# Optimization experiments

Hardware: AMD Instinct MI355X
Metric: run time of the kernel (lower is better)

The kernel has to match this reference:

```python
import jax, jax.numpy as jnp
import numpy as np

EPS = 1e-8

def _apply_norms(x):
    # x: [B, C, H, W]; torch .std() is unbiased (ddof=1)
    x_min = x.min(axis=1, keepdims=True)
    x_max = x.max(axis=1, keepdims=True)
    norm_minmax = (x - x_min) / (x_max - x_min + EPS)
    x_mean = x.mean(axis=1, keepdims=True)
    x_std = x.std(axis=1, keepdims=True, ddof=1)
    norm_z = (x - x_mean) / (x_std + EPS)
    b_mean = x.mean(axis=(0, 2, 3), keepdims=True)
    b_std = x.std(axis=(0, 2, 3), keepdims=True, ddof=1)
    norm_bn = (x - b_mean) / (b_std + EPS)
    return [norm_minmax, norm_z, norm_bn]

def _compute_metrics(pred, targ):
    B, C, H, W = pred.shape
    p = pred.reshape(B, C, H * W)
    t = targ.reshape(B, C, H * W)
    # SAM: 1 - cosine similarity over channel dim (torch clamps norms at eps)
    dot = (p * t).sum(axis=1)
    np_ = jnp.maximum(jnp.sqrt((p * p).sum(axis=1)), EPS)
    nt_ = jnp.maximum(jnp.sqrt((t * t).sum(axis=1)), EPS)
    sam = 1.0 - dot / (np_ * nt_)
    # Pearson over channel dim
    p_ctr = p - p.mean(axis=1, keepdims=True)
    t_ctr = t - t.mean(axis=1, keepdims=True)
    cov = (p_ctr * t_ctr).sum(axis=1)
    std_p = jnp.sqrt((p_ctr ** 2).sum(axis=1) + EPS)
    std_t = jnp.sqrt((t_ctr ** 2).sum(axis=1) + EPS)
    pearson = 1.0 - cov / (std_p * std_t)
    # SID: symmetric KL over channel-normalized positive distributions
    p_pos = p - p.min(axis=1, keepdims=True)
    t_pos = t - t.min(axis=1, keepdims=True)
    p_prob = jnp.maximum(p_pos / (p_pos.sum(axis=1, keepdims=True) + EPS), EPS)
    t_prob = jnp.maximum(t_pos / (t_pos.sum(axis=1, keepdims=True) + EPS), EPS)
    log_ratio = jnp.log(p_prob / t_prob)
    d_pt = (p_prob * log_ratio).sum(axis=1)
    d_tp = (t_prob * (-log_ratio)).sum(axis=1)
    sid = d_pt + d_tp
    return sam, pearson, sid  # each [B, H*W]

TOP_K_RATIO = 0.05

def setup_inputs() -> dict:
    key = jax.random.key(0)
    k1, k2 = jax.random.split(key)
    B, C, H, W = 4, 128, 256, 256
    reconstructed = jax.random.normal(k1, (B, C, H, W), dtype=jnp.float32)
    target = jax.random.normal(k2, (B, C, H, W), dtype=jnp.float32)
    loss_weights = jnp.ones((9,), dtype=jnp.float32)
    return {"reconstructed": reconstructed, "target": target, "loss_weights": loss_weights}

def reference(reconstructed, target, loss_weights):
    B, C, H, W = reconstructed.shape
    preds = _apply_norms(reconstructed)
    targs = _apply_norms(target)
    all_losses = []
    for p_norm, t_norm in zip(preds, targs):
        sam, pearson, sid = _compute_metrics(p_norm, t_norm)
        all_losses.extend([sam, pearson, sid])
    stacked = jnp.stack(all_losses, axis=0)  # [9, B, H*W]
    weights = jax.nn.softmax(loss_weights).reshape(9, 1, 1)
    weighted_error_map = (stacked * weights).sum(axis=0)  # [B, H*W]
    err_flat = weighted_error_map.reshape(-1)
    k = max(1, int(err_flat.shape[0] * TOP_K_RATIO))
    top_k_errors, _ = jax.lax.top_k(err_flat, k)
    return jnp.mean(top_k_errors), weighted_error_map.reshape(B, H, W)
```

## Files before the change

### kernel.cpp

```cpp
#include <hip/hip_runtime.h>

#define EPSF 1e-8f
#define CCH 128
#define HWSZ 65536
#define NPIX 262144
#define KTOP 13107
#define LN2F 0.6931471805599453f

#define WS_CST    512
#define WS_WGT    1024
#define WS_MINKEY 1040
#define WS_MAXKEY 1041
#define WS_BSTAR  1042
#define WS_CNTAB  1043
#define WS_LO2    1044
#define WS_W2     1045
#define WS_K2     1046
#define WS_SUMAB  1048
#define WS_H1     1056
#define WS_H2C    5152
#define WS_H2S    9248
#define WS_TOTAL  13344

__device__ __forceinline__ unsigned fkey(float f){
  unsigned u = __float_as_uint(f);
  return (u & 0x80000000u) ? ~u : (u | 0x80000000u);
}
__device__ __forceinline__ float funkey(unsigned k){
  unsigned u = (k & 0x80000000u) ? (k & 0x7fffffffu) : ~k;
  return __uint_as_float(u);
}

struct Stats {
  float psum,psumsq,tsum,tsumsq,ptsum,pmin,pmax,tmin,tmax;
  float bS1,bS11,bS2,bS22,bS12,bMp,bMt;
};
struct Consts { float errBase,fp,Bp,ft,Bt,fbp,Bbp,fbt,Bbt,sidW,bnW; };

__device__ Consts pixEpilogue(const Stats& s, const float* wgt){
  const float Ci = 1.0f/128.0f;
  float smm_p = 1.f/(s.pmax-s.pmin+EPSF);
  float smm_t = 1.f/(s.tmax-s.tmin+EPSF);
  float mean_p = s.psum*Ci, mean_t = s.tsum*Ci;
  float var_p = fmaxf((s.psumsq - s.psum*s.psum*Ci)*(1.f/127.f), 0.f);
  float var_t = fmaxf((s.tsumsq - s.tsum*s.tsum*Ci)*(1.f/127.f), 0.f);
  float zi_p = 1.f/(sqrtf(var_p)+EPSF);
  float zi_t = 1.f/(sqrtf(var_t)+EPSF);

  auto metrics = [&](float S1,float S11,float S2,float S22,float S12,
                     float& sam,float& pear){
    float npn = fmaxf(sqrtf(fmaxf(S11,0.f)), EPSF);
    float ntn = fmaxf(sqrtf(fmaxf(S22,0.f)), EPSF);
    sam = 1.f - S12/(npn*ntn);
    float cov = S12 - S1*S2*Ci;
    float vp = fmaxf(S11 - S1*S1*Ci, 0.f);
    float vt = fmaxf(S22 - S2*S2*Ci, 0.f);
    pear = 1.f - cov/(sqrtf(vp+EPSF)*sqrtf(vt+EPSF));
  };
  auto affine = [&](float ap,float sp,float at,float st,float& sam,float& pear){
    float S1 = (s.psum - 128.f*ap)*sp;
    float S11 = (s.psumsq - 2.f*ap*s.psum + 128.f*ap*ap)*sp*sp;
    float S2 = (s.tsum - 128.f*at)*st;
    float S22 = (s.tsumsq - 2.f*at*s.tsum + 128.f*at*at)*st*st;
    float S12 = (s.ptsum - at*s.psum - ap*s.tsum + 128.f*ap*at)*sp*st;
    metrics(S1,S11,S2,S22,S12,sam,pear);
  };

  float sam_mm,pear_mm,sam_z,pear_z,sam_bn,pear_bn;
  affine(s.pmin,smm_p,s.tmin,smm_t,sam_mm,pear_mm);
  affine(mean_p,zi_p,mean_t,zi_t,sam_z,pear_z);
  metrics(s.bS1,s.bS11,s.bS2,s.bS22,s.bS12,sam_bn,pear_bn);

  Consts c;
  c.errBase = wgt[0]*sam_mm + wgt[1]*pear_mm + wgt[3]*sam_z + wgt[4]*pear_z
            + wgt[6]*sam_bn + wgt[7]*pear_bn;
  float dp = fmaf(s.psum - 128.f*s.pmin, smm_p, EPSF);
  c.fp = smm_p/dp;  c.Bp = s.pmin*c.fp;
  float dt = fmaf(s.tsum - 128.f*s.tmin, smm_t, EPSF);
  c.ft = smm_t/dt;  c.Bt = s.tmin*c.ft;
  c.fbp = 1.f/((s.bS1 - 128.f*s.bMp) + EPSF); c.Bbp = s.bMp*c.fbp;
  c.fbt = 1.f/((s.bS2 - 128.f*s.bMt) + EPSF); c.Bbt = s.bMt*c.fbt;
  c.sidW = (wgt[2]+wgt[5])*LN2F;
  c.bnW  = wgt[8]*LN2F;
  return c;
}

__global__ __launch_bounds__(256) void initWs(unsigned* __restrict__ wsu){
  int idx = blockIdx.x*256 + threadIdx.x;
  if (idx < WS_TOTAL) wsu[idx] = (idx == WS_MINKEY) ? 0xFFFFFFFFu : 0u;
}

__global__ __launch_bounds__(256) void streamStatsKernel(const float* __restrict__ rec,
                                                         const float* __restrict__ tgt,
                                                         float* __restrict__ wsf){
  __shared__ float ws_[4], wq_[4];
  int tid = threadIdx.x;
  for (int ch = blockIdx.x; ch < 16384; ch += 2048){
    int tensor = ch >> 13;
    int ci = ch & 8191;
    const float4* base = (const float4*)(tensor ? tgt : rec) + (size_t)ci*1024;
    float4 L0 = base[tid];
    float4 L1 = base[tid + 256];
    float4 L2 = base[tid + 512];
    float4 L3 = base[tid + 768];
    float s = ((L0.x+L0.y)+(L0.z+L0.w)) + ((L1.x+L1.y)+(L1.z+L1.w))
            + ((L2.x+L2.y)+(L2.z+L2.w)) + ((L3.x+L3.y)+(L3.z+L3.w));
    float q = (fmaf(L0.x,L0.x,L0.y*L0.y) + fmaf(L0.z,L0.z,L0.w*L0.w))
            + (fmaf(L1.x,L1.x,L1.y*L1.y) + fmaf(L1.z,L1.z,L1.w*L1.w))
            + (fmaf(L2.x,L2.x,L2.y*L2.y) + fmaf(L2.z,L2.z,L2.w*L2.w))
            + (fmaf(L3.x,L3.x,L3.y*L3.y) + fmaf(L3.z,L3.z,L3.w*L3.w));
    #pragma unroll
    for (int off=1; off<64; off<<=1){ s += __shfl_xor(s,off); q += __shfl_xor(q,off); }
    int w = tid>>6;
    if ((tid&63)==0){ ws_[w]=s; wq_[w]=q; }
    __syncthreads();
    if (tid==0){
      float S = ws_[0]+ws_[1]+ws_[2]+ws_[3];
      float Q = wq_[0]+wq_[1]+wq_[2]+wq_[3];
      int c = (ci >> 4) & 127;
      int sh = blockIdx.x & 7;
      atomicAdd(&wsf[WS_H1 + sh*512 + tensor*256 + c], S);
      atomicAdd(&wsf[WS_H1 + sh*512 + tensor*256 + 128 + c], Q);
    }
    __syncthreads();
  }
}

__global__ __launch_bounds__(256) void finalizeKernel(const float* __restrict__ lw,
                                                      float* __restrict__ wsf){
  int tid = threadIdx.x;
  if (tid < 128){
    int c = tid;
    float sp=0,qp=0,st=0,qt=0;
    #pragma unroll
    for (int s=0;s<8;s++){
      const float* shp = wsf + WS_H1 + s*512;
      sp += shp[c];       qp += shp[128+c];
      st += shp[256+c];   qt += shp[384+c];
    }
    const float N = 262144.f;
    float mean_p = sp/N;
    float var_p = fmaxf((qp - sp*sp/N)/(N-1.f), 0.f);
    float inv_p = 1.f/(sqrtf(var_p)+EPSF);
    float mean_t = st/N;
    float var_t = fmaxf((qt - st*st/N)/(N-1.f), 0.f);
    float inv_t = 1.f/(sqrtf(var_t)+EPSF);
    wsf[WS_CST + c*4 + 0] = inv_p;
    wsf[WS_CST + c*4 + 1] = mean_p*inv_p;
    wsf[WS_CST + c*4 + 2] = inv_t;
    wsf[WS_CST + c*4 + 3] = mean_t*inv_t;
  }
  if (tid==0){
    float m = -1e30f;
    for (int i=0;i<9;i++) m = fmaxf(m, lw[i]);
    float e[9], sum=0.f;
    for (int i=0;i<9;i++){ e[i]=expf(lw[i]-m); sum+=e[i]; }
    for (int i=0;i<9;i++) wsf[WS_WGT+i] = e[i]/sum;
  }
  __syncthreads();
  for (int i=tid; i<4096; i+=256) wsf[WS_H1+i] = 0.f;
}

__global__ __launch_bounds__(256, 4) void mainKernel(const float* __restrict__ rec,
                                                     const float* __restrict__ tgt,
                                                     const float* __restrict__ wsf,
                                                     unsigned* __restrict__ wsu,
                                                     float* __restrict__ errMap){
  __shared__ float4 cst[128];
  __shared__ float wgtS[12];
  __shared__ float rmn[4], rmx[4];
  int tid = threadIdx.x;
  if (tid < 128) cst[tid] = ((const float4*)(wsf + WS_CST))[tid];
  if (tid < 9)  wgtS[tid] = wsf[WS_WGT + tid];
  __syncthreads();

  int pix0 = blockIdx.x*512 + tid*2;
  int b = pix0 >> 16;
  unsigned hwb = (unsigned)(pix0 & (HWSZ-1)) * 4u;
  const char* pB = (const char*)(rec + ((size_t)b*CCH)*HWSZ) + hwb;
  const char* tB = (const char*)(tgt + ((size_t)b*CCH)*HWSZ) + hwb;

  float2 psum={0,0},psumsq={0,0},tsum={0,0},tsumsq={0,0},ptsum={0,0};
  float2 pmin={3.4e38f,3.4e38f},pmax={-3.4e38f,-3.4e38f};
  float2 tmin={3.4e38f,3.4e38f},tmax={-3.4e38f,-3.4e38f};
  float2 bS1={0,0},bS11={0,0},bS2={0,0},bS22={0,0},bS12={0,0};
  float2 bMp={3.4e38f,3.4e38f},bMt={3.4e38f,3.4e38f};

  for (int cb=0; cb<CCH; cb+=8){
    float2 P[8], T[8];
    #pragma unroll
    for (int j=0;j<8;j++){
      P[j] = *(const float2*)(pB + ((unsigned)(cb+j)<<18));
      T[j] = *(const float2*)(tB + ((unsigned)(cb+j)<<18));
    }
    #pragma unroll
    for (int j=0;j<8;j++){
      asm volatile("" : "+v"(P[j].x), "+v"(P[j].y), "+v"(T[j].x), "+v"(T[j].y));
    }
    #pragma unroll
    for (int j=0;j<8;j++){
      float4 k = cst[cb+j];
      float2 pv=P[j], tv=T[j];
      psum.x+=pv.x; psum.y+=pv.y;
      psumsq.x=fmaf(pv.x,pv.x,psumsq.x); psumsq.y=fmaf(pv.y,pv.y,psumsq.y);
      tsum.x+=tv.x; tsum.y+=tv.y;
      tsumsq.x=fmaf(tv.x,tv.x,tsumsq.x); tsumsq.y=fmaf(tv.y,tv.y,tsumsq.y);
      ptsum.x=fmaf(pv.x,tv.x,ptsum.x); ptsum.y=fmaf(pv.y,tv.y,ptsum.y);
      pmin.x=fminf(pmin.x,pv.x); pmin.y=fminf(pmin.y,pv.y);
      pmax.x=fmaxf(pmax.x,pv.x); pmax.y=fmaxf(pmax.y,pv.y);
      tmin.x=fminf(tmin.x,tv.x); tmin.y=fminf(tmin.y,tv.y);
      tmax.x=fmaxf(tmax.x,tv.x); tmax.y=fmaxf(tmax.y,tv.y);
      float bpx = fmaf(pv.x,k.x,-k.y), bpy = fmaf(pv.y,k.x,-k.y);
      float btx = fmaf(tv.x,k.z,-k.w), bty = fmaf(tv.y,k.z,-k.w);
      bS1.x+=bpx; bS1.y+=bpy;
      bS11.x=fmaf(bpx,bpx,bS11.x); bS11.y=fmaf(bpy,bpy,bS11.y);
      bS2.x+=btx; bS2.y+=bty;
      bS22.x=fmaf(btx,btx,bS22.x); bS22.y=fmaf(bty,bty,bS22.y);
      bS12.x=fmaf(bpx,btx,bS12.x); bS12.y=fmaf(bpy,bty,bS12.y);
      bMp.x=fminf(bMp.x,bpx); bMp.y=fminf(bMp.y,bpy);
      bMt.x=fminf(bMt.x,btx); bMt.y=fminf(bMt.y,bty);
    }
  }

  Stats sx = {psum.x,psumsq.x,tsum.x,tsumsq.x,ptsum.x,pmin.x,pmax.x,tmin.x,tmax.x,
              bS1.x,bS11.x,bS2.x,bS22.x,bS12.x,bMp.x,bMt.x};
  Stats sy = {psum.y,psumsq.y,tsum.y,tsumsq.y,ptsum.y,pmin.y,pmax.y,tmin.y,tmax.y,
              bS1.y,bS11.y,bS2.y,bS22.y,bS12.y,bMp.y,bMt.y};
  Consts cx = pixEpilogue(sx, wgtS);
  Consts cy = pixEpilogue(sy, wgtS);

  float2 sid_mm={0,0}, sid_bn={0,0};
  for (int cb=0; cb<CCH; cb+=8){
    float2 P[8], T[8];
    #pragma unroll
    for (int j=0;j<8;j++){
      P[j] = *(const float2*)(pB + ((unsigned)(cb+j)<<18));
      T[j] = *(const float2*)(tB + ((unsigned)(cb+j)<<18));
    }
    #pragma unroll
    for (int j=0;j<8;j++){
      asm volatile("" : "+v"(P[j].x), "+v"(P[j].y), "+v"(T[j].x), "+v"(T[j].y));
    }
    #pragma unroll
    for (int j=0;j<8;j++){
      float4 k = cst[cb+j];
      float2 pv=P[j], tv=T[j];
      float ppx = fmaxf(fmaf(pv.x,cx.fp,-cx.Bp), EPSF);
      float tpx = fmaxf(fmaf(tv.x,cx.ft,-cx.Bt), EPSF);
      sid_mm.x = fmaf(ppx-tpx, __log2f(ppx)-__log2f(tpx), sid_mm.x);
      float ppy = fmaxf(fmaf(pv.y,cy.fp,-cy.Bp), EPSF);
      float tpy = fmaxf(fmaf(tv.y,cy.ft,-cy.Bt), EPSF);
      sid_mm.y = fmaf(ppy-tpy, __log2f(ppy)-__log2f(tpy), sid_mm.y);
      float bpx = fmaf(pv.x,k.x,-k.y), bpy = fmaf(pv.y,k.x,-k.y);
      float btx = fmaf(tv.x,k.z,-k.w), bty = fmaf(tv.y,k.z,-k.w);
      float qpx = fmaxf(fmaf(bpx,cx.fbp,-cx.Bbp), EPSF);
      float qtx = fmaxf(fmaf(btx,cx.fbt,-cx.Bbt), EPSF);
      sid_bn.x = fmaf(qpx-qtx, __log2f(qpx)-__log2f(qtx), sid_bn.x);
      float qpy = fmaf(bpy,cy.fbp,-cy.Bbp);  qpy = fmaxf(qpy, EPSF);
      float qty = fmaf(bty,cy.fbt,-cy.Bbt);  qty = fmaxf(qty, EPSF);
      sid_bn.y = fmaf(qpy-qty, __log2f(qpy)-__log2f(qty), sid_bn.y);
    }
  }

  float errx = cx.errBase + cx.sidW*sid_mm.x + cx.bnW*sid_bn.x;
  float erry = cy.errBase + cy.sidW*sid_mm.y + cy.bnW*sid_bn.y;
  errMap[pix0]   = errx;
  errMap[pix0+1] = erry;

  float emin = fminf(errx,erry), emax = fmaxf(errx,erry);
  #pragma unroll
  for (int off=1; off<64; off<<=1){
    emin = fminf(emin, __shfl_xor(emin,off));
    emax = fmaxf(emax, __shfl_xor(emax,off));
  }
  int w = tid>>6;
  if ((tid&63)==0){ rmn[w]=emin; rmx[w]=emax; }
  __syncthreads();
  if (tid==0){
    emin = fminf(fminf(rmn[0],rmn[1]),fminf(rmn[2],rmn[3]));
    emax = fmaxf(fmaxf(rmx[0],rmx[1]),fmaxf(rmx[2],rmx[3]));
    atomicMin(&wsu[WS_MINKEY], fkey(emin));
    atomicMax(&wsu[WS_MAXKEY], fkey(emax));
  }
}

__global__ __launch_bounds__(256) void hist1Kernel(const float* __restrict__ err,
                                                   unsigned* __restrict__ wsu){
  __shared__ unsigned h[4096];
  int tid = threadIdx.x;
  for (int i=tid;i<4096;i+=256) h[i]=0u;
  __syncthreads();
  float lo = funkey(wsu[WS_MINKEY]);
  float hi = funkey(wsu[WS_MAXKEY]);
  float invw = 4096.f / fmaxf(hi-lo, 1e-30f);
  int base = blockIdx.x*2048 + tid;
  for (int j=0;j<8;j++){
    float v = err[base + j*256];
    int idx = (int)fminf(fmaxf((v-lo)*invw, 0.f), 4095.f);
    atomicAdd(&h[idx], 1u);
  }
  __syncthreads();
  for (int i=tid;i<4096;i+=256){ unsigned c=h[i]; if (c) atomicAdd(&wsu[WS_H1+i], c); }
}

__global__ __launch_bounds__(256) void scan1Kernel(float* __restrict__ wsf,
                                                   unsigned* __restrict__ wsu){
  __shared__ unsigned counts[4096];
  __shared__ unsigned s[256];
  int tid = threadIdx.x;
  for (int i=tid;i<4096;i+=256) counts[i]=wsu[WS_H1+i];
  __syncthreads();
  unsigned part=0;
  for (int j=0;j<16;j++) part += counts[tid*16+j];
  s[tid]=part; __syncthreads();
  for (int off=1; off<256; off<<=1){
    unsigned v = (tid+off<256)? s[tid+off] : 0u;
    __syncthreads();
    s[tid] += v;
    __syncthreads();
  }
  float lo = funkey(wsu[WS_MINKEY]);
  float hi = funkey(wsu[WS_MAXKEY]);
  float w1 = fmaxf(hi-lo, 1e-30f) * (1.f/4096.f);
  unsigned cum = (tid<255)? s[tid+1] : 0u;
  for (int j=15;j>=0;j--){
    int bin = tid*16+j;
    unsigned cn = cum + counts[bin];
    if (cum < (unsigned)KTOP && cn >= (unsigned)KTOP){
      wsu[WS_BSTAR] = (unsigned)bin;
      wsu[WS_CNTAB] = cum;
      wsu[WS_K2]    = (unsigned)KTOP - cum;
      wsf[WS_LO2]   = lo + (float)bin*w1;
      wsf[WS_W2]    = w1*(1.f/4096.f);
    }
    cum = cn;
  }
}

__global__ __launch_bounds__(256) void hist2Kernel(const float* __restrict__ err,
                                                   float* __restrict__ wsf,
                                                   unsigned* __restrict__ wsu){
  __shared__ unsigned h2[4096];
  __shared__ float s2[4096];
  __shared__ float ls[4];
  int tid = threadIdx.x;
  for (int i=tid;i<4096;i+=256){ h2[i]=0u; s2[i]=0.f; }
  __syncthreads();
  float lo = funkey(wsu[WS_MINKEY]);
  float hi = funkey(wsu[WS_MAXKEY]);
  float invw = 4096.f / fmaxf(hi-lo, 1e-30f);
  int bstar = (int)wsu[WS_BSTAR];
  float lo2 = wsf[WS_LO2];
  float w2  = wsf[WS_W2];
  float invw2 = 1.f / w2;
  float mySum = 0.f;
  int base = blockIdx.x*2048 + tid;
  for (int j=0;j<8;j++){
    float v = err[base + j*256];
    int idx = (int)fminf(fmaxf((v-lo)*invw, 0.f), 4095.f);
    if (idx > bstar){
      mySum += v;
    } else if (idx == bstar){
      int i2 = (int)fminf(fmaxf((v-lo2)*invw2, 0.f), 4095.f);
      atomicAdd(&h2[i2], 1u);
      atomicAdd(&s2[i2], v);
    }
  }
  for (int off=1; off<64; off<<=1) mySum += __shfl_xor(mySum, off);
  if ((tid&63)==0) ls[tid>>6] = mySum;
  __syncthreads();
  if (tid==0) atomicAdd(&wsf[WS_SUMAB], ls[0]+ls[1]+ls[2]+ls[3]);
  for (int i=tid;i<4096;i+=256){
    unsigned c = h2[i]; if (c) atomicAdd(&wsu[WS_H2C+i], c);
    float sv = s2[i];   if (sv != 0.f) atomicAdd(&wsf[WS_H2S+i], sv);
  }
}

__global__ __launch_bounds__(256) void scan2Kernel(float* __restrict__ wsf,
                                                   unsigned* __restrict__ wsu,
                                                   float* __restrict__ out){
  __shared__ unsigned cnt[4096];
  __shared__ float sm[4096];
  __shared__ unsigned sC[256];
  __shared__ float sS[256];
  int tid = threadIdx.x;
  for (int i=tid;i<4096;i+=256){ cnt[i]=wsu[WS_H2C+i]; sm[i]=wsf[WS_H2S+i]; }
  __syncthreads();
  unsigned pc=0; float ps=0.f;
  for (int j=0;j<16;j++){ pc+=cnt[tid*16+j]; ps+=sm[tid*16+j]; }
  sC[tid]=pc; sS[tid]=ps; __syncthreads();
  for (int off=1; off<256; off<<=1){
    unsigned vc = (tid+off<256)? sC[tid+off] : 0u;
    float vs    = (tid+off<256)? sS[tid+off] : 0.f;
    __syncthreads();
    sC[tid] += vc; sS[tid] += vs;
    __syncthreads();
  }
  unsigned k2 = wsu[WS_K2];
  float lo2 = wsf[WS_LO2], w2 = wsf[WS_W2];
  unsigned cum = (tid<255)? sC[tid+1] : 0u;
  float cums   = (tid<255)? sS[tid+1] : 0.f;
  for (int j=15;j>=0;j--){
    int bin = tid*16+j;
    unsigned cn = cum + cnt[bin];
    float sn = cums + sm[bin];
    if (cum < k2 && cn >= k2){
      float val = lo2 + ((float)bin + 0.5f)*w2;
      float total = wsf[WS_SUMAB] + cums + (float)(k2 - cum)*val;
      out[0] = total / (float)KTOP;
    }
    cum = cn; cums = sn;
  }
}

extern "C" void kernel_launch(void* const* d_in, const int* in_sizes, int n_in,
                              void* d_out, int out_size, void* d_ws, size_t ws_size,
                              hipStream_t stream){
  const float* rec = (const float*)d_in[0];
  const float* tgt = (const float*)d_in[1];
  const float* lw  = (const float*)d_in[2];
  float* out = (float*)d_out;
  float* wsf = (float*)d_ws;
  unsigned* wsu = (unsigned*)d_ws;

  hipLaunchKernelGGL(initWs, dim3((WS_TOTAL+255)/256), dim3(256), 0, stream, wsu);
  hipLaunchKernelGGL(streamStatsKernel, dim3(2048), dim3(256), 0, stream, rec, tgt, wsf);
  hipLaunchKernelGGL(finalizeKernel, dim3(1), dim3(256), 0, stream, lw, wsf);
  hipLaunchKernelGGL(mainKernel, dim3(NPIX/512), dim3(256), 0, stream, rec, tgt, wsf, wsu, out+1);
  hipLaunchKernelGGL(hist1Kernel, dim3(128), dim3(256), 0, stream, out+1, wsu);
  hipLaunchKernelGGL(scan1Kernel, dim3(1), dim3(256), 0, stream, wsf, wsu);
  hipLaunchKernelGGL(hist2Kernel, dim3(128), dim3(256), 0, stream, out+1, wsf, wsu);
  hipLaunchKernelGGL(scan2Kernel, dim3(1), dim3(256), 0, stream, wsf, wsu, out);
}
```

Measured before the change: 167.3 us.

## Restructure per-channel stats kernel for many independent strided loads per thread

Replaces the chunk-looped stats kernel, which did a block-wide reduction with __syncthreads per 16KB chunk, with one where each thread issues 16 strided float4 loads per tensor, grouped 8 at a time behind an asm barrier so the loads stay in flight together. Each thread covers four channels in separate accumulators, so only wave-level shuffles are needed, with no shared memory or block barriers. The aim is more memory-level parallelism and less synchronisation in this bandwidth-bound pass. In exchange it uses more registers and issues more atomics per wave.

```diff
diff --git a/kernel.cpp b/kernel.cpp
--- a/kernel.cpp
+++ b/kernel.cpp
@@ -90,39 +90,54 @@
   if (idx < WS_TOTAL) wsu[idx] = (idx == WS_MINKEY) ? 0xFFFFFFFFu : 0u;
 }
 
-__global__ __launch_bounds__(256) void streamStatsKernel(const float* __restrict__ rec,
-                                                         const float* __restrict__ tgt,
-                                                         float* __restrict__ wsf){
-  __shared__ float ws_[4], wq_[4];
-  int tid = threadIdx.x;
-  for (int ch = blockIdx.x; ch < 16384; ch += 2048){
-    int tensor = ch >> 13;
-    int ci = ch & 8191;
-    const float4* base = (const float4*)(tensor ? tgt : rec) + (size_t)ci*1024;
-    float4 L0 = base[tid];
-    float4 L1 = base[tid + 256];
-    float4 L2 = base[tid + 512];
-    float4 L3 = base[tid + 768];
-    float s = ((L0.x+L0.y)+(L0.z+L0.w)) + ((L1.x+L1.y)+(L1.z+L1.w))
-            + ((L2.x+L2.y)+(L2.z+L2.w)) + ((L3.x+L3.y)+(L3.z+L3.w));
-    float q = (fmaf(L0.x,L0.x,L0.y*L0.y) + fmaf(L0.z,L0.z,L0.w*L0.w))
-            + (fmaf(L1.x,L1.x,L1.y*L1.y) + fmaf(L1.z,L1.z,L1.w*L1.w))
-            + (fmaf(L2.x,L2.x,L2.y*L2.y) + fmaf(L2.z,L2.z,L2.w*L2.w))
-            + (fmaf(L3.x,L3.x,L3.y*L3.y) + fmaf(L3.z,L3.z,L3.w*L3.w));
-    #pragma unroll
-    for (int off=1; off<64; off<<=1){ s += __shfl_xor(s,off); q += __shfl_xor(q,off); }
-    int w = tid>>6;
-    if ((tid&63)==0){ ws_[w]=s; wq_[w]=q; }
-    __syncthreads();
-    if (tid==0){
-      float S = ws_[0]+ws_[1]+ws_[2]+ws_[3];
-      float Q = wq_[0]+wq_[1]+wq_[2]+wq_[3];
-      int c = (ci >> 4) & 127;
-      int sh = blockIdx.x & 7;
-      atomicAdd(&wsf[WS_H1 + sh*512 + tensor*256 + c], S);
-      atomicAdd(&wsf[WS_H1 + sh*512 + tensor*256 + 128 + c], Q);
-    }
-    __syncthreads();
+__global__ __launch_bounds__(256) void statsKernel(const float* __restrict__ rec,
+                                                   const float* __restrict__ tgt,
+                                                   float* __restrict__ wsf){
+  int tid = threadIdx.x;
+  int g0 = blockIdx.x*256 + tid;
+  int c0 = (g0 >> 14) & 127;
+  int lane = tid & 63;
+  int sh = (blockIdx.x & 7)*512;
+
+  #pragma unroll
+  for (int tensor=0; tensor<2; tensor++){
+    const float4* S = (const float4*)(tensor ? tgt : rec);
+    float s0=0,s1=0,s2=0,s3=0,q0=0,q1=0,q2=0,q3=0;
+    #pragma unroll
+    for (int kb=0; kb<16; kb+=8){
+      float4 L[8];
+      #pragma unroll
+      for (int j=0;j<8;j++) L[j] = S[(size_t)g0 + (size_t)(kb+j)*524288];
+      #pragma unroll
+      for (int j=0;j<8;j++)
+        asm volatile("" : "+v"(L[j].x), "+v"(L[j].y), "+v"(L[j].z), "+v"(L[j].w));
+      #pragma unroll
+      for (int j=0;j<8;j+=4){
+        float4 a=L[j], b=L[j+1], c=L[j+2], d=L[j+3];
+        s0 += (a.x+a.y)+(a.z+a.w); q0 += fmaf(a.x,a.x,a.y*a.y)+fmaf(a.z,a.z,a.w*a.w);
+        s1 += (b.x+b.y)+(b.z+b.w); q1 += fmaf(b.x,b.x,b.y*b.y)+fmaf(b.z,b.z,b.w*b.w);
+        s2 += (c.x+c.y)+(c.z+c.w); q2 += fmaf(c.x,c.x,c.y*c.y)+fmaf(c.z,c.z,c.w*c.w);
+        s3 += (d.x+d.y)+(d.z+d.w); q3 += fmaf(d.x,d.x,d.y*d.y)+fmaf(d.z,d.z,d.w*d.w);
+      }
+    }
+    #pragma unroll
+    for (int off=1; off<64; off<<=1){
+      s0+=__shfl_xor(s0,off); s1+=__shfl_xor(s1,off);
+      s2+=__shfl_xor(s2,off); s3+=__shfl_xor(s3,off);
+      q0+=__shfl_xor(q0,off); q1+=__shfl_xor(q1,off);
+      q2+=__shfl_xor(q2,off); q3+=__shfl_xor(q3,off);
+    }
+    if (lane==0){
+      int base = WS_H1 + sh + tensor*256;
+      atomicAdd(&wsf[base + c0], s0);
+      atomicAdd(&wsf[base + ((c0+32)&127)], s1);
+      atomicAdd(&wsf[base + ((c0+64)&127)], s2);
+      atomicAdd(&wsf[base + ((c0+96)&127)], s3);
+      atomicAdd(&wsf[base + 128 + c0], q0);
+      atomicAdd(&wsf[base + 128 + ((c0+32)&127)], q1);
+      atomicAdd(&wsf[base + 128 + ((c0+64)&127)], q2);
+      atomicAdd(&wsf[base + 128 + ((c0+96)&127)], q3);
+    }
   }
 }
 
@@ -424,7 +439,7 @@
   unsigned* wsu = (unsigned*)d_ws;
 
   hipLaunchKernelGGL(initWs, dim3((WS_TOTAL+255)/256), dim3(256), 0, stream, wsu);
-  hipLaunchKernelGGL(streamStatsKernel, dim3(2048), dim3(256), 0, stream, rec, tgt, wsf);
+  hipLaunchKernelGGL(statsKernel, dim3(2048), dim3(256), 0, stream, rec, tgt, wsf);
   hipLaunchKernelGGL(finalizeKernel, dim3(1), dim3(256), 0, stream, lw, wsf);
   hipLaunchKernelGGL(mainKernel, dim3(NPIX/512), dim3(256), 0, stream, rec, tgt, wsf, wsu, out+1);
   hipLaunchKernelGGL(hist1Kernel, dim3(128), dim3(256), 0, stream, out+1, wsu);
```

Result: slower. 171.8 us (+2.7%).
